# Performance work log

Hardware: AMD Instinct MI355X
Metric: run time of the kernel (lower is better)

## Reference

```python
import jax, jax.numpy as jnp
import numpy as np

T, D, E, K, F, SF = 4096, 1024, 8, 2, 1024, 1024  # tokens, d_model, experts, top_k, moe_ff, shared_ff


def setup_inputs() -> dict:
    key = jax.random.key(0)
    ks = jax.random.split(key, 10)
    hidden_states = jax.random.normal(ks[0], (T, D), jnp.float32)
    # balanced expert assignment: the fused kernel's get_split_sizes assumes tokens
    # split evenly across experts after permute_tokens, so exactly T*K/E per expert
    flat = jnp.arange(T * K) % E
    flat = jax.random.permutation(ks[1], flat)
    topk_indices = flat.reshape(T, K).astype(jnp.int32)
    w = jax.random.uniform(ks[2], (T, K), jnp.float32)
    topk_weights = w / w.sum(-1, keepdims=True)  # norm_topk_prob
    s = 0.02
    w_gate = jax.random.normal(ks[3], (E, D, F), jnp.float32) * s
    w_up = jax.random.normal(ks[4], (E, D, F), jnp.float32) * s
    w_down = jax.random.normal(ks[5], (E, F, D), jnp.float32) * s
    sw_gate = jax.random.normal(ks[6], (D, SF), jnp.float32) * s
    sw_up = jax.random.normal(ks[7], (D, SF), jnp.float32) * s
    sw_down = jax.random.normal(ks[8], (SF, D), jnp.float32) * s
    shared_gate_w = jax.random.normal(ks[9], (D, 1), jnp.float32) * s
    return dict(hidden_states=hidden_states, topk_weights=topk_weights,
                w_gate=w_gate, w_up=w_up, w_down=w_down,
                sw_gate=sw_gate, sw_up=sw_up, sw_down=sw_down,
                shared_gate_w=shared_gate_w, topk_indices=topk_indices)


def _silu(x):
    return x * jax.nn.sigmoid(x)


def reference(hidden_states, topk_weights, w_gate, w_up, w_down,
              sw_gate, sw_up, sw_down, shared_gate_w, topk_indices):
    t, d = hidden_states.shape
    e = w_gate.shape[0]
    k = topk_indices.shape[1]
    c = (t * k) // e  # tokens per expert (balanced split, as in get_split_sizes)

    # permute_tokens: replicate each token top_k times and sort by expert id
    flat_idx = topk_indices.reshape(-1)                    # [t*k]
    order = jnp.argsort(flat_idx)                          # dispatch permutation
    x_rep = jnp.repeat(hidden_states, k, axis=0)           # [t*k, d]
    xs = x_rep[order].reshape(e, c, d)                     # grouped per-expert

    # per-expert gated MLP (grouped GEMMs)
    h = _silu(jnp.einsum('ecd,edf->ecf', xs, w_gate)) * jnp.einsum('ecd,edf->ecf', xs, w_up)
    y = jnp.einsum('ecf,efd->ecd', h, w_down).reshape(t * k, d)

    # unpermute_tokens + weighted combine over top_k
    y = y[jnp.argsort(order)].reshape(t, k, d)
    out = (y * topk_weights[..., None]).sum(axis=1)        # [t, d]

    # shared expert with sigmoid gate
    s = jnp.einsum('tf,fd->td', _silu(hidden_states @ sw_gate) * (hidden_states @ sw_up), sw_down)
    g = jax.nn.sigmoid(hidden_states @ shared_gate_w)      # [t, 1]
    return (out + g * s).astype(hidden_states.dtype)
```

## Files before the change

kernel.cpp:

```cpp
#include <hip/hip_runtime.h>
#include <hip/hip_bf16.h>
#include <cstdint>
#include <cstddef>

#define TTOK 4096
#define DM   1024
#define NE   8
#define KTOP 2
#define FFD  1024
#define CPER 1024
#define MROWS 12288

typedef __attribute__((ext_vector_type(8))) short frag8;
typedef __attribute__((ext_vector_type(4))) float f32x4;

static __device__ __forceinline__ unsigned short f2bf(float f) {
  unsigned int u = __float_as_uint(f);
  u += 0x7fff + ((u >> 16) & 1);
  return (unsigned short)(u >> 16);
}
static __device__ __forceinline__ float bf2f(unsigned short u) {
  return __uint_as_float((unsigned int)u << 16);
}

static __device__ __forceinline__ void gld_lds16(const unsigned short* g, unsigned short* l) {
  __builtin_amdgcn_global_load_lds(
      (const __attribute__((address_space(1))) unsigned int*)g,
      (__attribute__((address_space(3))) unsigned int*)l,
      16, 0, 0);
}

static __device__ __forceinline__ int lds_slot(int r, int cs) {
  return r * 4 + (cs ^ ((r >> 1) & 3));
}

static __device__ __forceinline__ void stage_tile(const unsigned short* __restrict__ src,
                                                  int row0, int k0,
                                                  unsigned short* lds, int tid) {
#pragma unroll
  for (int it = 0; it < 2; ++it) {
    int seg = it * 256 + tid;
    int r = seg >> 2;
    int cs = (seg & 3) ^ ((r >> 1) & 3);
    gld_lds16(src + (size_t)(row0 + r) * 1024 + k0 + cs * 8, lds + seg * 8);
  }
}

static __device__ __forceinline__ void swizzle_xy(int& x, int& y) {
  int L = blockIdx.y * 8 + blockIdx.x;
  int xcd = L & 7;
  int s = L >> 3;
  y = xcd * 12 + s % 12;
  x = s / 12;
}

__global__ void perm_kernel(const int* __restrict__ idx, const float* __restrict__ tw,
                            int* __restrict__ cnt, int* __restrict__ rowsrc,
                            int* __restrict__ inv, float* __restrict__ rowscale) {
  int i = blockIdx.x * 256 + threadIdx.x;
  int e = idx[i];
  int pos = atomicAdd(&cnt[e], 1);
  int j = e * CPER + pos;
  rowsrc[j] = i >> 1;
  rowscale[j] = tw[i];
  inv[i] = j;
  if (i < TTOK) rowsrc[8192 + i] = i;
}

__global__ void conv_gate_kernel(const float* __restrict__ x, const float* __restrict__ gw,
                                 float* __restrict__ rowscale,
                                 unsigned short* __restrict__ xb) {
  int row = blockIdx.x * 4 + (threadIdx.x >> 6);
  int lane = threadIdx.x & 63;
  const float4* xr = (const float4*)(x + (size_t)row * 1024);
  const float4* wr = (const float4*)gw;
  ushort4* ob = (ushort4*)(xb + (size_t)row * 1024);
  float s = 0.f;
#pragma unroll
  for (int c = 0; c < 4; ++c) {
    int k = lane + 64 * c;
    float4 v = xr[k];
    float4 g = wr[k];
    s += v.x * g.x + v.y * g.y + v.z * g.z + v.w * g.w;
    ushort4 o;
    o.x = f2bf(v.x); o.y = f2bf(v.y); o.z = f2bf(v.z); o.w = f2bf(v.w);
    ob[k] = o;
  }
#pragma unroll
  for (int off = 32; off; off >>= 1) s += __shfl_down(s, off);
  if (lane == 0) rowscale[8192 + row] = 1.f / (1.f + __expf(-s));
}

__global__ void transw_kernel(const float* __restrict__ wg, const float* __restrict__ wu,
                              const float* __restrict__ wd, const float* __restrict__ sg,
                              const float* __restrict__ su, const float* __restrict__ sd,
                              unsigned short* __restrict__ owg, unsigned short* __restrict__ owu,
                              unsigned short* __restrict__ owd) {
  int z = blockIdx.z;
  const float* src; unsigned short* dst;
  if (z < 8)       { src = wg + (size_t)z * 1048576;        dst = owg + (size_t)z * 1048576; }
  else if (z < 16) { src = wu + (size_t)(z - 8) * 1048576;  dst = owu + (size_t)(z - 8) * 1048576; }
  else if (z < 24) { src = wd + (size_t)(z - 16) * 1048576; dst = owd + (size_t)(z - 16) * 1048576; }
  else if (z == 24){ src = sg; dst = owg + (size_t)8 * 1048576; }
  else if (z == 25){ src = su; dst = owu + (size_t)8 * 1048576; }
  else             { src = sd; dst = owd + (size_t)8 * 1048576; }
  __shared__ float tile[64][65];
  int bx = blockIdx.x * 64;
  int by = blockIdx.y * 64;
  int c4 = threadIdx.x & 15;
  int r0 = threadIdx.x >> 4;
#pragma unroll
  for (int i = 0; i < 4; ++i) {
    int r = r0 + 16 * i;
    float4 v = *(const float4*)&src[(size_t)(by + r) * 1024 + bx + c4 * 4];
    tile[r][c4 * 4 + 0] = v.x; tile[r][c4 * 4 + 1] = v.y;
    tile[r][c4 * 4 + 2] = v.z; tile[r][c4 * 4 + 3] = v.w;
  }
  __syncthreads();
#pragma unroll
  for (int i = 0; i < 4; ++i) {
    int f = r0 + 16 * i;
    ushort4 o;
    o.x = f2bf(tile[c4 * 4 + 0][f]);
    o.y = f2bf(tile[c4 * 4 + 1][f]);
    o.z = f2bf(tile[c4 * 4 + 2][f]);
    o.w = f2bf(tile[c4 * 4 + 3][f]);
    *(ushort4*)&dst[(size_t)(bx + f) * 1024 + by + c4 * 4] = o;
  }
}

static __device__ __forceinline__ int eid_of(int y) { return (y < 64) ? (y >> 3) : 8; }

__global__ __launch_bounds__(256, 2) void gemm1_kernel(
    const unsigned short* __restrict__ A, const int* __restrict__ rowsrc,
    const unsigned short* __restrict__ Bg, const unsigned short* __restrict__ Bu,
    unsigned short* __restrict__ H) {
  __shared__ __align__(16) unsigned short As[128 * 32];
  __shared__ __align__(16) unsigned short Bgs[128 * 32];
  __shared__ __align__(16) unsigned short Bus[128 * 32];
  int tid = threadIdx.x;
  int bx, by;
  swizzle_xy(bx, by);
  int e = eid_of(by);
  int row0 = by * 128;
  int col0 = bx * 128;
  const unsigned short* Bge = Bg + (size_t)e * 1048576;
  const unsigned short* Bue = Bu + (size_t)e * 1048576;

  int sA0 = tid, sA1 = 256 + tid;
  int rA0 = sA0 >> 2, rA1 = sA1 >> 2;
  int cA0 = (sA0 & 3) ^ ((rA0 >> 1) & 3);
  int cA1 = (sA1 & 3) ^ ((rA1 >> 1) & 3);
  const unsigned short* pA0 = A + (size_t)rowsrc[row0 + rA0] * 1024 + cA0 * 8;
  const unsigned short* pA1 = A + (size_t)rowsrc[row0 + rA1] * 1024 + cA1 * 8;

  int wave = tid >> 6, lane = tid & 63;
  int wm = wave >> 1, wn = wave & 1;
  int lr = lane & 15, q = lane >> 4;

  f32x4 accg[4][4], accu[4][4];
#pragma unroll
  for (int i = 0; i < 4; ++i)
#pragma unroll
    for (int j = 0; j < 4; ++j) {
      accg[i][j] = (f32x4){0.f, 0.f, 0.f, 0.f};
      accu[i][j] = (f32x4){0.f, 0.f, 0.f, 0.f};
    }

  for (int kt = 0; kt < 1024; kt += 32) {
    gld_lds16(pA0 + kt, As + sA0 * 8);
    gld_lds16(pA1 + kt, As + sA1 * 8);
    stage_tile(Bge, col0, kt, Bgs, tid);
    stage_tile(Bue, col0, kt, Bus, tid);
    __syncthreads();
    frag8 a[4], b0[4], b1[4];
#pragma unroll
    for (int i = 0; i < 4; ++i) {
      int r = wm * 64 + i * 16 + lr;
      a[i] = *(const frag8*)&As[lds_slot(r, q) * 8];
    }
#pragma unroll
    for (int j = 0; j < 4; ++j) {
      int r = wn * 64 + j * 16 + lr;
      b0[j] = *(const frag8*)&Bgs[lds_slot(r, q) * 8];
      b1[j] = *(const frag8*)&Bus[lds_slot(r, q) * 8];
    }
#pragma unroll
    for (int i = 0; i < 4; ++i)
#pragma unroll
      for (int j = 0; j < 4; ++j) {
        accg[i][j] = __builtin_amdgcn_mfma_f32_16x16x32_bf16(a[i], b0[j], accg[i][j], 0, 0, 0);
        accu[i][j] = __builtin_amdgcn_mfma_f32_16x16x32_bf16(a[i], b1[j], accu[i][j], 0, 0, 0);
      }
    __syncthreads();
  }
#pragma unroll
  for (int i = 0; i < 4; ++i)
#pragma unroll
    for (int j = 0; j < 4; ++j)
#pragma unroll
      for (int r = 0; r < 4; ++r) {
        int m = row0 + wm * 64 + i * 16 + q * 4 + r;
        int n = col0 + wn * 64 + j * 16 + lr;
        float gv = accg[i][j][r];
        float hv = gv / (1.f + __expf(-gv)) * accu[i][j][r];
        H[(size_t)m * 1024 + n] = f2bf(hv);
      }
}

__global__ __launch_bounds__(256, 2) void gemm2_kernel(
    const unsigned short* __restrict__ A, const unsigned short* __restrict__ B,
    const float* __restrict__ rowscale, unsigned short* __restrict__ Y) {
  __shared__ __align__(16) unsigned short As[128 * 32];
  __shared__ __align__(16) unsigned short Bs[128 * 32];
  int tid = threadIdx.x;
  int bx, by;
  swizzle_xy(bx, by);
  int e = eid_of(by);
  int row0 = by * 128;
  int col0 = bx * 128;
  const unsigned short* Be = B + (size_t)e * 1048576;

  int wave = tid >> 6, lane = tid & 63;
  int wm = wave >> 1, wn = wave & 1;
  int lr = lane & 15, q = lane >> 4;

  f32x4 acc[4][4];
#pragma unroll
  for (int i = 0; i < 4; ++i)
#pragma unroll
    for (int j = 0; j < 4; ++j) acc[i][j] = (f32x4){0.f, 0.f, 0.f, 0.f};

  for (int kt = 0; kt < 1024; kt += 32) {
    stage_tile(A, row0, kt, As, tid);
    stage_tile(Be, col0, kt, Bs, tid);
    __syncthreads();
    frag8 a[4], b[4];
#pragma unroll
    for (int i = 0; i < 4; ++i) {
      int r = wm * 64 + i * 16 + lr;
      a[i] = *(const frag8*)&As[lds_slot(r, q) * 8];
    }
#pragma unroll
    for (int j = 0; j < 4; ++j) {
      int r = wn * 64 + j * 16 + lr;
      b[j] = *(const frag8*)&Bs[lds_slot(r, q) * 8];
    }
#pragma unroll
    for (int i = 0; i < 4; ++i)
#pragma unroll
      for (int j = 0; j < 4; ++j)
        acc[i][j] = __builtin_amdgcn_mfma_f32_16x16x32_bf16(a[i], b[j], acc[i][j], 0, 0, 0);
    __syncthreads();
  }
#pragma unroll
  for (int i = 0; i < 4; ++i)
#pragma unroll
    for (int r = 0; r < 4; ++r) {
      int m = row0 + wm * 64 + i * 16 + q * 4 + r;
      float sc = rowscale[m];
#pragma unroll
      for (int j = 0; j < 4; ++j) {
        int n = col0 + wn * 64 + j * 16 + lr;
        Y[(size_t)m * 1024 + n] = f2bf(sc * acc[i][j][r]);
      }
    }
}

__global__ void combine_kernel(const unsigned short* __restrict__ Y,
                               const int* __restrict__ inv, float* __restrict__ out) {
  int base = blockIdx.x * 256 + threadIdx.x;
#pragma unroll
  for (int k = 0; k < 2; ++k) {
    int slot = base + k * 524288;
    int t = slot >> 8;
    int c = slot & 255;
    int j0 = inv[2 * t], j1 = inv[2 * t + 1];
    ushort4 a = ((const ushort4*)(Y + (size_t)j0 * 1024))[c];
    ushort4 b = ((const ushort4*)(Y + (size_t)j1 * 1024))[c];
    ushort4 s = ((const ushort4*)(Y + (size_t)(8192 + t) * 1024))[c];
    float4 o;
    o.x = bf2f(a.x) + bf2f(b.x) + bf2f(s.x);
    o.y = bf2f(a.y) + bf2f(b.y) + bf2f(s.y);
    o.z = bf2f(a.z) + bf2f(b.z) + bf2f(s.z);
    o.w = bf2f(a.w) + bf2f(b.w) + bf2f(s.w);
    ((float4*)(out + (size_t)t * 1024))[c] = o;
  }
}

extern "C" void kernel_launch(void* const* d_in, const int* in_sizes, int n_in,
                              void* d_out, int out_size, void* d_ws, size_t ws_size,
                              hipStream_t stream) {
  (void)in_sizes; (void)n_in; (void)out_size; (void)ws_size;
  const float* hidden  = (const float*)d_in[0];
  const float* topk_w  = (const float*)d_in[1];
  const float* w_gate  = (const float*)d_in[2];
  const float* w_up    = (const float*)d_in[3];
  const float* w_down  = (const float*)d_in[4];
  const float* sw_gate = (const float*)d_in[5];
  const float* sw_up   = (const float*)d_in[6];
  const float* sw_down = (const float*)d_in[7];
  const float* sgw     = (const float*)d_in[8];
  const int*   topk_i  = (const int*)d_in[9];
  float* out = (float*)d_out;

  char* p = (char*)d_ws;
  auto alloc = [&](size_t bytes) {
    char* r = p;
    p += (bytes + 255) & ~(size_t)255;
    return r;
  };
  unsigned short* Wg_all = (unsigned short*)alloc((size_t)9 * 1048576 * 2);
  unsigned short* Wu_all = (unsigned short*)alloc((size_t)9 * 1048576 * 2);
  unsigned short* Wd_all = (unsigned short*)alloc((size_t)9 * 1048576 * 2);
  unsigned short* Xbf    = (unsigned short*)alloc((size_t)TTOK * 1024 * 2);
  unsigned short* Hall   = (unsigned short*)alloc((size_t)MROWS * 1024 * 2);
  unsigned short* Yall   = (unsigned short*)alloc((size_t)MROWS * 1024 * 2);
  int*   cnt      = (int*)alloc(NE * 4);
  int*   rowsrc   = (int*)alloc((size_t)MROWS * 4);
  int*   inv      = (int*)alloc((size_t)TTOK * KTOP * 4);
  float* rowscale = (float*)alloc((size_t)MROWS * 4);

  hipMemsetAsync(cnt, 0, NE * 4, stream);

  perm_kernel<<<TTOK * KTOP / 256, 256, 0, stream>>>(topk_i, topk_w, cnt, rowsrc, inv, rowscale);
  conv_gate_kernel<<<TTOK / 4, 256, 0, stream>>>(hidden, sgw, rowscale, Xbf);
  transw_kernel<<<dim3(16, 16, 27), 256, 0, stream>>>(
      w_gate, w_up, w_down, sw_gate, sw_up, sw_down, Wg_all, Wu_all, Wd_all);

  gemm1_kernel<<<dim3(8, 96), 256, 0, stream>>>(Xbf, rowsrc, Wg_all, Wu_all, Hall);
  gemm2_kernel<<<dim3(8, 96), 256, 0, stream>>>(Hall, Wd_all, rowscale, Yall);
  combine_kernel<<<2048, 256, 0, stream>>>(Yall, inv, out);
}
```

Measured before the change: 312.3 us.

## Double GEMM K-tile to 64 with new swizzle and fuse perm into conversion kernel

Both grouped GEMMs now stage 64-wide K tiles in LDS instead of 32, with a new XOR swizzle over 8 column slots. This halves the number of barrier pairs per K loop and issues more loads per stage. It also doubles LDS use per block, which may limit occupancy, especially in gemm1 with three 16 KB buffers. Separately, the permutation kernel is merged into the bf16 conversion/gate kernel to remove one launch.

New measurement: 297.0 us. 1.05x faster.

```diff
diff --git a/kernel.cpp b/kernel.cpp
--- a/kernel.cpp
+++ b/kernel.cpp
@@ -30,18 +30,18 @@
       16, 0, 0);
 }
 
-static __device__ __forceinline__ int lds_slot(int r, int cs) {
-  return r * 4 + (cs ^ ((r >> 1) & 3));
-}
-
-static __device__ __forceinline__ void stage_tile(const unsigned short* __restrict__ src,
-                                                  int row0, int k0,
-                                                  unsigned short* lds, int tid) {
-#pragma unroll
-  for (int it = 0; it < 2; ++it) {
+static __device__ __forceinline__ int lds_slot64(int r, int c) {
+  return r * 8 + (c ^ (r & 7));
+}
+
+static __device__ __forceinline__ void stage_tile64(const unsigned short* __restrict__ src,
+                                                    int row0, int k0,
+                                                    unsigned short* lds, int tid) {
+#pragma unroll
+  for (int it = 0; it < 4; ++it) {
     int seg = it * 256 + tid;
-    int r = seg >> 2;
-    int cs = (seg & 3) ^ ((r >> 1) & 3);
+    int r = seg >> 3;
+    int cs = (seg & 7) ^ (r & 7);
     gld_lds16(src + (size_t)(row0 + r) * 1024 + k0 + cs * 8, lds + seg * 8);
   }
 }
@@ -54,22 +54,21 @@
   x = s / 12;
 }
 
-__global__ void perm_kernel(const int* __restrict__ idx, const float* __restrict__ tw,
+__global__ void prep_kernel(const float* __restrict__ x, const float* __restrict__ gw,
+                            const int* __restrict__ idx, const float* __restrict__ tw,
                             int* __restrict__ cnt, int* __restrict__ rowsrc,
-                            int* __restrict__ inv, float* __restrict__ rowscale) {
-  int i = blockIdx.x * 256 + threadIdx.x;
-  int e = idx[i];
-  int pos = atomicAdd(&cnt[e], 1);
-  int j = e * CPER + pos;
-  rowsrc[j] = i >> 1;
-  rowscale[j] = tw[i];
-  inv[i] = j;
-  if (i < TTOK) rowsrc[8192 + i] = i;
-}
-
-__global__ void conv_gate_kernel(const float* __restrict__ x, const float* __restrict__ gw,
-                                 float* __restrict__ rowscale,
-                                 unsigned short* __restrict__ xb) {
+                            int* __restrict__ inv, float* __restrict__ rowscale,
+                            unsigned short* __restrict__ xb) {
+  if (blockIdx.x < 32) {
+    int i = blockIdx.x * 256 + threadIdx.x;
+    int e = idx[i];
+    int pos = atomicAdd(&cnt[e], 1);
+    int j = e * CPER + pos;
+    rowsrc[j] = i >> 1;
+    rowscale[j] = tw[i];
+    inv[i] = j;
+    if (i < TTOK) rowsrc[8192 + i] = i;
+  }
   int row = blockIdx.x * 4 + (threadIdx.x >> 6);
   int lane = threadIdx.x & 63;
   const float4* xr = (const float4*)(x + (size_t)row * 1024);
@@ -135,9 +134,9 @@
     const unsigned short* __restrict__ A, const int* __restrict__ rowsrc,
     const unsigned short* __restrict__ Bg, const unsigned short* __restrict__ Bu,
     unsigned short* __restrict__ H) {
-  __shared__ __align__(16) unsigned short As[128 * 32];
-  __shared__ __align__(16) unsigned short Bgs[128 * 32];
-  __shared__ __align__(16) unsigned short Bus[128 * 32];
+  __shared__ __align__(16) unsigned short As[128 * 64];
+  __shared__ __align__(16) unsigned short Bgs[128 * 64];
+  __shared__ __align__(16) unsigned short Bus[128 * 64];
   int tid = threadIdx.x;
   int bx, by;
   swizzle_xy(bx, by);
@@ -147,12 +146,14 @@
   const unsigned short* Bge = Bg + (size_t)e * 1048576;
   const unsigned short* Bue = Bu + (size_t)e * 1048576;
 
-  int sA0 = tid, sA1 = 256 + tid;
-  int rA0 = sA0 >> 2, rA1 = sA1 >> 2;
-  int cA0 = (sA0 & 3) ^ ((rA0 >> 1) & 3);
-  int cA1 = (sA1 & 3) ^ ((rA1 >> 1) & 3);
-  const unsigned short* pA0 = A + (size_t)rowsrc[row0 + rA0] * 1024 + cA0 * 8;
-  const unsigned short* pA1 = A + (size_t)rowsrc[row0 + rA1] * 1024 + cA1 * 8;
+  const unsigned short* pA[4];
+#pragma unroll
+  for (int it = 0; it < 4; ++it) {
+    int seg = it * 256 + tid;
+    int r = seg >> 3;
+    int cs = (seg & 7) ^ (r & 7);
+    pA[it] = A + (size_t)rowsrc[row0 + r] * 1024 + cs * 8;
+  }
 
   int wave = tid >> 6, lane = tid & 63;
   int wm = wave >> 1, wn = wave & 1;
@@ -167,31 +168,36 @@
       accu[i][j] = (f32x4){0.f, 0.f, 0.f, 0.f};
     }
 
-  for (int kt = 0; kt < 1024; kt += 32) {
-    gld_lds16(pA0 + kt, As + sA0 * 8);
-    gld_lds16(pA1 + kt, As + sA1 * 8);
-    stage_tile(Bge, col0, kt, Bgs, tid);
-    stage_tile(Bue, col0, kt, Bus, tid);
+  for (int kt = 0; kt < 1024; kt += 64) {
+#pragma unroll
+    for (int it = 0; it < 4; ++it)
+      gld_lds16(pA[it] + kt, As + (it * 256 + tid) * 8);
+    stage_tile64(Bge, col0, kt, Bgs, tid);
+    stage_tile64(Bue, col0, kt, Bus, tid);
     __syncthreads();
-    frag8 a[4], b0[4], b1[4];
-#pragma unroll
-    for (int i = 0; i < 4; ++i) {
-      int r = wm * 64 + i * 16 + lr;
-      a[i] = *(const frag8*)&As[lds_slot(r, q) * 8];
+#pragma unroll
+    for (int kk = 0; kk < 2; ++kk) {
+      int c = kk * 4 + q;
+      frag8 a[4], b0[4], b1[4];
+#pragma unroll
+      for (int i = 0; i < 4; ++i) {
+        int r = wm * 64 + i * 16 + lr;
+        a[i] = *(const frag8*)&As[lds_slot64(r, c) * 8];
+      }
+#pragma unroll
+      for (int j = 0; j < 4; ++j) {
+        int r = wn * 64 + j * 16 + lr;
+        b0[j] = *(const frag8*)&Bgs[lds_slot64(r, c) * 8];
+        b1[j] = *(const frag8*)&Bus[lds_slot64(r, c) * 8];
+      }
+#pragma unroll
+      for (int i = 0; i < 4; ++i)
+#pragma unroll
+        for (int j = 0; j < 4; ++j) {
+          accg[i][j] = __builtin_amdgcn_mfma_f32_16x16x32_bf16(a[i], b0[j], accg[i][j], 0, 0, 0);
+          accu[i][j] = __builtin_amdgcn_mfma_f32_16x16x32_bf16(a[i], b1[j], accu[i][j], 0, 0, 0);
+        }
     }
-#pragma unroll
-    for (int j = 0; j < 4; ++j) {
-      int r = wn * 64 + j * 16 + lr;
-      b0[j] = *(const frag8*)&Bgs[lds_slot(r, q) * 8];
-      b1[j] = *(const frag8*)&Bus[lds_slot(r, q) * 8];
-    }
-#pragma unroll
-    for (int i = 0; i < 4; ++i)
-#pragma unroll
-      for (int j = 0; j < 4; ++j) {
-        accg[i][j] = __builtin_amdgcn_mfma_f32_16x16x32_bf16(a[i], b0[j], accg[i][j], 0, 0, 0);
-        accu[i][j] = __builtin_amdgcn_mfma_f32_16x16x32_bf16(a[i], b1[j], accu[i][j], 0, 0, 0);
-      }
     __syncthreads();
   }
 #pragma unroll
@@ -211,8 +217,8 @@
 __global__ __launch_bounds__(256, 2) void gemm2_kernel(
     const unsigned short* __restrict__ A, const unsigned short* __restrict__ B,
     const float* __restrict__ rowscale, unsigned short* __restrict__ Y) {
-  __shared__ __align__(16) unsigned short As[128 * 32];
-  __shared__ __align__(16) unsigned short Bs[128 * 32];
+  __shared__ __align__(16) unsigned short As[128 * 64];
+  __shared__ __align__(16) unsigned short Bs[128 * 64];
   int tid = threadIdx.x;
   int bx, by;
   swizzle_xy(bx, by);
@@ -231,26 +237,30 @@
 #pragma unroll
     for (int j = 0; j < 4; ++j) acc[i][j] = (f32x4){0.f, 0.f, 0.f, 0.f};
 
-  for (int kt = 0; kt < 1024; kt += 32) {
-    stage_tile(A, row0, kt, As, tid);
-    stage_tile(Be, col0, kt, Bs, tid);
+  for (int kt = 0; kt < 1024; kt += 64) {
+    stage_tile64(A, row0, kt, As, tid);
+    stage_tile64(Be, col0, kt, Bs, tid);
     __syncthreads();
-    frag8 a[4], b[4];
-#pragma unroll
-    for (int i = 0; i < 4; ++i) {
-      int r = wm * 64 + i * 16 + lr;
-      a[i] = *(const frag8*)&As[lds_slot(r, q) * 8];
+#pragma unroll
+    for (int kk = 0; kk < 2; ++kk) {
+      int c = kk * 4 + q;
+      frag8 a[4], b[4];
+#pragma unroll
+      for (int i = 0; i < 4; ++i) {
+        int r = wm * 64 + i * 16 + lr;
+        a[i] = *(const frag8*)&As[lds_slot64(r, c) * 8];
+      }
+#pragma unroll
+      for (int j = 0; j < 4; ++j) {
+        int r = wn * 64 + j * 16 + lr;
+        b[j] = *(const frag8*)&Bs[lds_slot64(r, c) * 8];
+      }
+#pragma unroll
+      for (int i = 0; i < 4; ++i)
+#pragma unroll
+        for (int j = 0; j < 4; ++j)
+          acc[i][j] = __builtin_amdgcn_mfma_f32_16x16x32_bf16(a[i], b[j], acc[i][j], 0, 0, 0);
     }
-#pragma unroll
-    for (int j = 0; j < 4; ++j) {
-      int r = wn * 64 + j * 16 + lr;
-      b[j] = *(const frag8*)&Bs[lds_slot(r, q) * 8];
-    }
-#pragma unroll
-    for (int i = 0; i < 4; ++i)
-#pragma unroll
-      for (int j = 0; j < 4; ++j)
-        acc[i][j] = __builtin_amdgcn_mfma_f32_16x16x32_bf16(a[i], b[j], acc[i][j], 0, 0, 0);
     __syncthreads();
   }
 #pragma unroll
@@ -323,8 +333,8 @@
 
   hipMemsetAsync(cnt, 0, NE * 4, stream);
 
-  perm_kernel<<<TTOK * KTOP / 256, 256, 0, stream>>>(topk_i, topk_w, cnt, rowsrc, inv, rowscale);
-  conv_gate_kernel<<<TTOK / 4, 256, 0, stream>>>(hidden, sgw, rowscale, Xbf);
+  prep_kernel<<<TTOK / 4, 256, 0, stream>>>(hidden, sgw, topk_i, topk_w,
+                                            cnt, rowsrc, inv, rowscale, Xbf);
   transw_kernel<<<dim3(16, 16, 27), 256, 0, stream>>>(
       w_gate, w_up, w_down, sw_gate, sw_up, sw_down, Wg_all, Wu_all, Wd_all);
 
```
